# Kernel optimization log

Measured on AMD Instinct MI355X. Metric: run time of the kernel, lower is better.

Reference implementation:

```python
import jax, jax.numpy as jnp
import numpy as np

LN_EPS = 1e-5

def _layer_norm(y, g, b):
    mu = y.mean(-1, keepdims=True)
    var = y.var(-1, keepdims=True)
    return (y - mu) * jax.lax.rsqrt(var + LN_EPS) * g + b

def setup_inputs() -> dict:
    key = jax.random.key(0)
    ks = jax.random.split(key, 10)
    F, D, H = 32, 128, 128
    FD = F * D
    B = 8192
    def rn(k, shape, fan_in):
        return jax.random.normal(k, shape, dtype=jnp.float32) / np.sqrt(fan_in)
    return {
        "x":   jax.random.normal(ks[0], (B, F), dtype=jnp.float32),
        "Wp":  rn(ks[1], (F, D), 1), "bp": jnp.zeros((F, D), jnp.float32),
        "fW1": rn(ks[2], (F, D, H), D), "fb1": jnp.zeros((F, H), jnp.float32),
        "fW2": rn(ks[3], (F, H, D), H), "fb2": jnp.zeros((F, D), jnp.float32),
        "fWg": rn(ks[4], (F, D, 2 * D), D), "fbg": jnp.zeros((F, 2 * D), jnp.float32),
        "fg":  jnp.ones((F, D), jnp.float32), "fbe": jnp.zeros((F, D), jnp.float32),
        "sW1": rn(ks[5], (FD, H), FD), "sb1": jnp.zeros((H,), jnp.float32),
        "sW2": rn(ks[6], (H, FD), H), "sb2": jnp.zeros((FD,), jnp.float32),
        "sWg": rn(ks[7], (FD, 2 * FD), FD), "sbg": jnp.zeros((2 * FD,), jnp.float32),
        "sg":  jnp.ones((FD,), jnp.float32), "sbe": jnp.zeros((FD,), jnp.float32),
        "Wh":  rn(ks[8], (FD, F), FD), "bh": jnp.zeros((F,), jnp.float32),
    }

def reference(x, Wp, bp, fW1, fb1, fW2, fb2, fWg, fbg, fg, fbe,
              sW1, sb1, sW2, sb2, sWg, sbg, sg, sbe, Wh, bh):
    B, F = x.shape
    D = Wp.shape[1]
    # per-feature Linear(1, d_model), batched over all features: (B, F, D)
    emb = x[:, :, None] * Wp[None] + bp[None]
    # per-feature GRNs, batched via einsum over the feature axis
    h = jax.nn.elu(jnp.einsum('bfd,fdh->bfh', emb, fW1) + fb1)
    h = jnp.einsum('bfh,fhd->bfd', h, fW2) + fb2
    gates = jnp.einsum('bfd,fde->bfe', h, fWg) + fbg          # (B, F, 2D)
    a, s = jnp.split(gates, 2, axis=-1)
    stacked = _layer_norm(emb + a * jax.nn.sigmoid(s), fg, fbe)  # (B, F, D)
    # selection GRN over the flattened embeddings
    flat = stacked.reshape(B, F * D)
    hh = jax.nn.elu(flat @ sW1 + sb1)
    hh = hh @ sW2 + sb2
    sgate = flat_gate = hh @ sWg + sbg                          # (B, 2FD)
    sa, ss = jnp.split(sgate, 2, axis=-1)
    sel_in = _layer_norm(flat + sa * jax.nn.sigmoid(ss), sg, sbe)
    weights = jax.nn.softmax(sel_in @ Wh + bh, axis=-1)        # (B, F)
    selected = jnp.einsum('bfd,bf->bd', stacked, weights)      # (B, D)
    return selected, weights
```

## Files before the change

### kernel.cpp

```cpp
#include <hip/hip_runtime.h>
#include <hip/hip_bf16.h>
#include <math.h>

#define BB 8192
#define FF 32
#define DD 128
#define HH 128
#define FD 4096
#define E2 256
#define F2 8192
#define LN_EPS 1e-5f
#define L2E 1.44269504f
#define KSPLIT 8

typedef __hip_bfloat16 bf16;
typedef __attribute__((ext_vector_type(8))) short bf16x8;
typedef __attribute__((ext_vector_type(4))) float f32x4;

__device__ __forceinline__ float s2f(short s) {
  union { float f; unsigned u; } x; x.u = ((unsigned)(unsigned short)s) << 16; return x.f;
}
__device__ __forceinline__ short f2s(float v) {
  bf16 h = __float2bfloat16(v); return *(short*)&h;
}
__device__ __forceinline__ float fast_sigmoid(float s) {
  return __builtin_amdgcn_rcpf(1.f + __builtin_amdgcn_exp2f(-L2E * s));
}
__device__ __forceinline__ float fast_elu(float v) {
  return v > 0.f ? v : __builtin_amdgcn_exp2f(L2E * v) - 1.f;
}

__device__ __forceinline__ int swz64(int row, int hb) {
  return row * 128 + (hb ^ ((row & 7) << 4));
}


__global__ void prep_A1(const float* __restrict__ Wp, const float* __restrict__ bp,
                        const float* __restrict__ fW1, const float* __restrict__ fb1,
                        float* __restrict__ A1, float* __restrict__ C1) {
  int f = blockIdx.x, h = threadIdx.x;
  const float* w1 = fW1 + (size_t)f * DD * HH;
  float a = 0.f, c = 0.f;
  for (int d = 0; d < DD; ++d) {
    float w = w1[d * HH + h];
    a += Wp[f * DD + d] * w;
    c += bp[f * DD + d] * w;
  }
  A1[f * HH + h] = a;
  C1[f * HH + h] = c + fb1[f * HH + h];
}

__global__ void prep_M2(const float* __restrict__ fW2, const float* __restrict__ fWg,
                        float* __restrict__ M2) {
  int f = blockIdx.x, h = blockIdx.y, e = threadIdx.x;
  const float* w2 = fW2 + ((size_t)f * HH + h) * DD;
  const float* wg = fWg + (size_t)f * DD * E2;
  float acc = 0.f;
  for (int d = 0; d < DD; ++d) acc += w2[d] * wg[d * E2 + e];
  M2[((size_t)f * HH + h) * E2 + e] = acc;
}

__global__ void m2_castT(const float* __restrict__ M2, short* __restrict__ M2T) {
  __shared__ float T[64][65];
  int h0 = blockIdx.x * 64, e0 = blockIdx.y * 64, f = blockIdx.z;
  int t = threadIdx.x;
  for (int i = 0; i < 4; ++i) {
    int lin = t + 256 * i;
    int r = lin >> 4, c4 = (lin & 15) * 4;
    f32x4 v = *(const f32x4*)&M2[((size_t)f * HH + h0 + r) * E2 + e0 + c4];
    T[r][c4] = v[0]; T[r][c4 + 1] = v[1]; T[r][c4 + 2] = v[2]; T[r][c4 + 3] = v[3];
  }
  __syncthreads();
  for (int i = 0; i < 2; ++i) {
    int lin = t + 256 * i;
    int e = lin >> 3, h8 = (lin & 7) * 8;
    short o[8];
    for (int k = 0; k < 8; ++k) o[k] = f2s(T[h8 + k][e]);
    *(bf16x8*)&M2T[((size_t)f * E2 + e0 + e) * HH + h0 + h8] = *(bf16x8*)&o[0];
  }
}

__global__ void prep_c2(const float* __restrict__ fb2, const float* __restrict__ fWg,
                        const float* __restrict__ fbg, float* __restrict__ c2) {
  int f = blockIdx.x, e = threadIdx.x;
  const float* wg = fWg + (size_t)f * DD * E2;
  float acc = 0.f;
  for (int d = 0; d < DD; ++d) acc += fb2[f * DD + d] * wg[d * E2 + e];
  c2[f * E2 + e] = acc + fbg[f * E2 + e];
}

__global__ void cast_bf16(const float* __restrict__ in, short* __restrict__ out, int n) {
  int i = blockIdx.x * 256 + threadIdx.x;
  if (i < n) out[i] = f2s(in[i]);
}

__global__ void castT(const float* __restrict__ in, short* __restrict__ out, int R, int C) {
  __shared__ float T[64][65];
  int c0 = blockIdx.x * 64, r0 = blockIdx.y * 64;
  int t = threadIdx.x;
  for (int i = 0; i < 4; ++i) {
    int lin = t + 256 * i;
    int r = lin >> 4, c4 = (lin & 15) * 4;
    f32x4 v = *(const f32x4*)&in[(size_t)(r0 + r) * C + c0 + c4];
    T[r][c4] = v[0]; T[r][c4 + 1] = v[1]; T[r][c4 + 2] = v[2]; T[r][c4 + 3] = v[3];
  }
  __syncthreads();
  for (int i = 0; i < 2; ++i) {
    int lin = t + 256 * i;
    int c = lin >> 3, r8 = (lin & 7) * 8;
    short o[8];
    for (int e = 0; e < 8; ++e) o[e] = f2s(T[r8 + e][c]);
    *(bf16x8*)&out[(size_t)(c0 + c) * R + r0 + r8] = *(bf16x8*)&o[0];
  }
}

__global__ void init_misc(const float* __restrict__ sbg, const float* __restrict__ bh,
                          float* __restrict__ c3, float* __restrict__ rowstats,
                          float* __restrict__ u, float* __restrict__ w0) {
  int j = blockIdx.x * 256 + threadIdx.x;
  c3[j] = sbg[j];
  rowstats[2 * j] = 0.f;
  rowstats[2 * j + 1] = 0.f;
  if (j < 32) { u[j] = 0.f; w0[j] = bh[j]; }
}

__global__ void castT_c3(const float* __restrict__ in, short* __restrict__ out,
                         const float* __restrict__ sb2, float* __restrict__ c3) {
  __shared__ float T[64][65];
  int c0 = blockIdx.x * 64, r0 = blockIdx.y * 64;
  int t = threadIdx.x;
  for (int i = 0; i < 4; ++i) {
    int lin = t + 256 * i;
    int r = lin >> 4, c4 = (lin & 15) * 4;
    f32x4 v = *(const f32x4*)&in[(size_t)(r0 + r) * F2 + c0 + c4];
    T[r][c4] = v[0]; T[r][c4 + 1] = v[1]; T[r][c4 + 2] = v[2]; T[r][c4 + 3] = v[3];
  }
  __syncthreads();
  for (int i = 0; i < 2; ++i) {
    int lin = t + 256 * i;
    int c = lin >> 3, r8 = (lin & 7) * 8;
    short o[8];
    for (int e = 0; e < 8; ++e) o[e] = f2s(T[r8 + e][c]);
    *(bf16x8*)&out[(size_t)(c0 + c) * FD + r0 + r8] = *(bf16x8*)&o[0];
  }
  if (t < 64) {
    float s = 0.f;
    for (int r = 0; r < 64; ++r) s += sb2[r0 + r] * T[r][t];
    atomicAdd(&c3[c0 + t], s);
  }
}

__global__ void prep_whs(const float* __restrict__ Wh, const float* __restrict__ sg,
                         const float* __restrict__ sbe, short* __restrict__ WhS,
                         float* __restrict__ u, float* __restrict__ w0) {
  __shared__ float T[64][33];
  int k0 = blockIdx.x * 64;
  int t = threadIdx.x;
  {
    int k = t >> 5, c = t & 31;
    for (int i = 0; i < 8; ++i)
      T[k + 8 * i][c] = Wh[(size_t)(k0 + k + 8 * i) * FF + c];
  }
  __syncthreads();
  {
    int c = t >> 3, kk = (t & 7) * 8;
    short o[8];
    for (int i = 0; i < 8; ++i) o[i] = f2s(sg[k0 + kk + i] * T[kk + i][c]);
    *(bf16x8*)&WhS[(size_t)c * FD + k0 + kk] = *(bf16x8*)&o[0];
  }
  if (t < 32) {
    float su = 0.f, sw = 0.f;
    for (int k = 0; k < 64; ++k) { su += sg[k0 + k] * T[k][t]; sw += sbe[k0 + k] * T[k][t]; }
    atomicAdd(&u[t], su);
    atomicAdd(&w0[t], sw);
  }
}

__global__ __launch_bounds__(256) void gemm_bt_n128_splitk(
    const short* __restrict__ A, const short* __restrict__ BT,
    float* __restrict__ Cp, int M, int K) {
  __shared__ short As[128 * 72];
  __shared__ short Bs[128 * 72];
  int m0 = blockIdx.x * 128;
  int kchunk = K >> 3;
  int kbase = blockIdx.y * kchunk;
  int tid = threadIdx.x;
  int lane = tid & 63, w = tid >> 6;
  int wm = (w >> 1) * 64, wn = (w & 1) * 64;
  int lm = lane & 15, lq = lane >> 4;
  f32x4 acc[4][4] = {};
  for (int kc = 0; kc < kchunk; kc += 64) {
    for (int i = 0; i < 4; ++i) {
      int li = tid + 256 * i;
      int r = li >> 3, c8 = (li & 7) * 8;
      *(bf16x8*)&As[r * 72 + c8] = *(const bf16x8*)&A[(size_t)(m0 + r) * K + kbase + kc + c8];
      *(bf16x8*)&Bs[r * 72 + c8] = *(const bf16x8*)&BT[(size_t)r * K + kbase + kc + c8];
    }
    __syncthreads();
    for (int ks = 0; ks < 2; ++ks) {
      bf16x8 af[4], bfr[4];
      for (int i = 0; i < 4; ++i)
        af[i] = *(const bf16x8*)&As[(wm + i * 16 + lm) * 72 + ks * 32 + lq * 8];
      for (int j = 0; j < 4; ++j)
        bfr[j] = *(const bf16x8*)&Bs[(wn + j * 16 + lm) * 72 + ks * 32 + lq * 8];
      for (int i = 0; i < 4; ++i)
        for (int j = 0; j < 4; ++j)
          acc[i][j] = __builtin_amdgcn_mfma_f32_16x16x32_bf16(af[i], bfr[j], acc[i][j], 0, 0, 0);
    }
    __syncthreads();
  }
  float* out = Cp + (size_t)blockIdx.y * M * 128;
  for (int i = 0; i < 4; ++i)
    for (int j = 0; j < 4; ++j)
      for (int v = 0; v < 4; ++v) {
        int r = wm + i * 16 + lq * 4 + v;
        int c = wn + j * 16 + lm;
        out[(size_t)(m0 + r) * 128 + c] = acc[i][j][v];
      }
}

__global__ void reduce_m3t(const float* __restrict__ Cp, short* __restrict__ M3T, int M) {
  size_t i = (size_t)blockIdx.x * 256 + threadIdx.x;
  float s = 0.f;
  for (int k = 0; k < KSPLIT; ++k) s += Cp[(size_t)k * M * 128 + i];
  M3T[i] = f2s(s);
}

__global__ void reduce_hh1(const float* __restrict__ Cp, const float* __restrict__ sb1,
                           short* __restrict__ hh1, int M) {
  size_t i = (size_t)blockIdx.x * 256 + threadIdx.x;
  float s = 0.f;
  for (int k = 0; k < KSPLIT; ++k) s += Cp[(size_t)k * M * 128 + i];
  s += sb1[i & 127];
  hh1[i] = f2s(fast_elu(s));
}

__global__ __launch_bounds__(256) void stageA_mfma(
    const float* __restrict__ x, const float* __restrict__ Wp,
    const float* __restrict__ bp, const float* __restrict__ A1,
    const float* __restrict__ C1, const short* __restrict__ M2T,
    const float* __restrict__ c2, const float* __restrict__ fg,
    const float* __restrict__ fbe, short* __restrict__ stacked) {
  __shared__ __align__(16) char SM[(64 + 128) * 128];
  char* As = SM;
  char* Bs = SM + 64 * 128;
  short* Co = (short*)(SM + 64 * 128);
  float* red = (float*)SM;
  __shared__ float xsh[64];
  int f = blockIdx.y;
  int m0 = blockIdx.x * 64;
  int tid = threadIdx.x;
  int lane = tid & 63, w = tid >> 6;
  int wm = (w >> 1) * 32, wn = (w & 1) * 64;
  int lm = lane & 15, lq = lane >> 4;
  if (tid < 64) xsh[tid] = x[(size_t)(m0 + tid) * FF + f];
  __syncthreads();
  f32x4 accA[2][4] = {}, accB[2][4] = {};
  int c8 = (tid & 7) * 8, rb = tid >> 3;
  for (int kc = 0; kc < HH; kc += 64) {
    {
      f32x4 a1lo = *(const f32x4*)&A1[f * HH + kc + c8];
      f32x4 a1hi = *(const f32x4*)&A1[f * HH + kc + c8 + 4];
      f32x4 c1lo = *(const f32x4*)&C1[f * HH + kc + c8];
      f32x4 c1hi = *(const f32x4*)&C1[f * HH + kc + c8 + 4];
      for (int rr = 0; rr < 2; ++rr) {
        int row = rb + rr * 32;
        float xr = xsh[row];
        short o[8];
        for (int e = 0; e < 4; ++e) {
          o[e]     = f2s(fast_elu(fmaf(xr, a1lo[e], c1lo[e])));
          o[e + 4] = f2s(fast_elu(fmaf(xr, a1hi[e], c1hi[e])));
        }
        *(bf16x8*)(As + swz64(row, c8 * 2)) = *(bf16x8*)&o[0];
      }
    }
    for (int i = 0; i < 4; ++i) {
      int li = tid + 256 * i;
      int r = li >> 3, cc = (li & 7) * 8;
      bf16x8 va = *(const bf16x8*)&M2T[((size_t)f * E2 + r) * HH + kc + cc];
      *(bf16x8*)(Bs + swz64(r, cc * 2)) = va;
    }
    __syncthreads();
    bf16x8 af[2][2];
    for (int ks = 0; ks < 2; ++ks)
      for (int i = 0; i < 2; ++i)
        af[ks][i] = *(const bf16x8*)(As + swz64(wm + i * 16 + lm, ks * 64 + lq * 16));
    for (int ks = 0; ks < 2; ++ks) {
      int hb = ks * 64 + lq * 16;
      for (int j = 0; j < 4; ++j) {
        bf16x8 ba = *(const bf16x8*)(Bs + swz64(wn + j * 16 + lm, hb));
        for (int i = 0; i < 2; ++i)
          accA[i][j] = __builtin_amdgcn_mfma_f32_16x16x32_bf16(af[ks][i], ba, accA[i][j], 0, 0, 0);
      }
    }
    __syncthreads();
    for (int i = 0; i < 4; ++i) {
      int li = tid + 256 * i;
      int r = li >> 3, cc = (li & 7) * 8;
      bf16x8 vb = *(const bf16x8*)&M2T[((size_t)f * E2 + 128 + r) * HH + kc + cc];
      *(bf16x8*)(Bs + swz64(r, cc * 2)) = vb;
    }
    __syncthreads();
    for (int ks = 0; ks < 2; ++ks) {
      int hb = ks * 64 + lq * 16;
      for (int j = 0; j < 4; ++j) {
        bf16x8 bb = *(const bf16x8*)(Bs + swz64(wn + j * 16 + lm, hb));
        for (int i = 0; i < 2; ++i)
          accB[i][j] = __builtin_amdgcn_mfma_f32_16x16x32_bf16(af[ks][i], bb, accB[i][j], 0, 0, 0);
      }
    }
    __syncthreads();
  }
  float c2a[4], c2s[4], wpv[4], bpv[4];
  for (int j = 0; j < 4; ++j) {
    int c = wn + j * 16 + lm;
    c2a[j] = c2[f * E2 + c];
    c2s[j] = c2[f * E2 + 128 + c];
    wpv[j] = Wp[f * DD + c];
    bpv[j] = bp[f * DD + c];
  }
  float rs[2][4], rq[2][4];
  for (int i = 0; i < 2; ++i)
    for (int v = 0; v < 4; ++v) {
      int r = wm + i * 16 + lq * 4 + v;
      float xr = xsh[r];
      float sum = 0.f, sq = 0.f;
      for (int j = 0; j < 4; ++j) {
        float a = accA[i][j][v] + c2a[j];
        float s = accB[i][j][v] + c2s[j];
        float emb = fmaf(xr, wpv[j], bpv[j]);
        float y = fmaf(a, fast_sigmoid(s), emb);
        accA[i][j][v] = y;
        sum += y; sq += y * y;
      }
      rs[i][v] = sum; rq[i][v] = sq;
    }
  for (int m = 1; m < 16; m <<= 1)
    for (int i = 0; i < 2; ++i)
      for (int v = 0; v < 4; ++v) {
        rs[i][v] += __shfl_xor(rs[i][v], m, 64);
        rq[i][v] += __shfl_xor(rq[i][v], m, 64);
      }
  if (lm == 0)
    for (int i = 0; i < 2; ++i)
      for (int v = 0; v < 4; ++v) {
        int r = wm + i * 16 + lq * 4 + v;
        red[(w & 1) * 128 + r * 2]     = rs[i][v];
        red[(w & 1) * 128 + r * 2 + 1] = rq[i][v];
      }
  __syncthreads();
  float fgv[4], fbev[4];
  for (int j = 0; j < 4; ++j) {
    int c = wn + j * 16 + lm;
    fgv[j] = fg[f * DD + c];
    fbev[j] = fbe[f * DD + c];
  }
  for (int i = 0; i < 2; ++i)
    for (int v = 0; v < 4; ++v) {
      int r = wm + i * 16 + lq * 4 + v;
      float tot  = red[r * 2]     + red[128 + r * 2];
      float totq = red[r * 2 + 1] + red[128 + r * 2 + 1];
      float mu = tot * (1.f / DD);
      float var = totq * (1.f / DD) - mu * mu;
      float rstd = rsqrtf(var + LN_EPS);
      for (int j = 0; j < 4; ++j) {
        int c = wn + j * 16 + lm;
        Co[r * 128 + c] = f2s((accA[i][j][v] - mu) * rstd * fgv[j] + fbev[j]);
      }
    }
  __syncthreads();
  for (int i = 0; i < 4; ++i) {
    int lin = tid + 256 * i;
    int r = lin >> 4, cc8 = (lin & 15) * 8;
    *(bf16x8*)&stacked[((size_t)(m0 + r) * FF + f) * DD + cc8] = *(bf16x8*)&Co[r * 128 + cc8];
  }
}

__global__ __launch_bounds__(256) void sgate_mfma(
    const short* __restrict__ hh1, const short* __restrict__ M3T,
    const float* __restrict__ c3, const short* __restrict__ stacked,
    short* __restrict__ tmp, float* __restrict__ rowstats) {
  __shared__ short As[128 * 72];
  __shared__ short Ba[64 * 72];
  __shared__ short Bb[64 * 72];
  short* Co = As;
  int m0 = blockIdx.x * 128;
  int c0 = blockIdx.y * 64;
  int tid = threadIdx.x;
  int lane = tid & 63, w = tid >> 6;
  int wm = (w >> 1) * 64, wn = (w & 1) * 32;
  int lm = lane & 15, lq = lane >> 4;
  f32x4 accA[4][2] = {}, accB[4][2] = {};
  for (int kc = 0; kc < 128; kc += 64) {
    for (int i = 0; i < 4; ++i) {
      int li = tid + 256 * i;
      int r = li >> 3, c8 = (li & 7) * 8;
      *(bf16x8*)&As[r * 72 + c8] = *(const bf16x8*)&hh1[(size_t)(m0 + r) * 128 + kc + c8];
    }
    for (int i = 0; i < 2; ++i) {
      int li = tid + 256 * i;
      int r = li >> 3, c8 = (li & 7) * 8;
      *(bf16x8*)&Ba[r * 72 + c8] = *(const bf16x8*)&M3T[(size_t)(c0 + r) * 128 + kc + c8];
      *(bf16x8*)&Bb[r * 72 + c8] = *(const bf16x8*)&M3T[(size_t)(4096 + c0 + r) * 128 + kc + c8];
    }
    __syncthreads();
    for (int ks = 0; ks < 2; ++ks) {
      bf16x8 af[4], ba[2], bb[2];
      for (int i = 0; i < 4; ++i)
        af[i] = *(const bf16x8*)&As[(wm + i * 16 + lm) * 72 + ks * 32 + lq * 8];
      for (int j = 0; j < 2; ++j) {
        ba[j] = *(const bf16x8*)&Ba[(wn + j * 16 + lm) * 72 + ks * 32 + lq * 8];
        bb[j] = *(const bf16x8*)&Bb[(wn + j * 16 + lm) * 72 + ks * 32 + lq * 8];
      }
      for (int i = 0; i < 4; ++i)
        for (int j = 0; j < 2; ++j) {
          accA[i][j] = __builtin_amdgcn_mfma_f32_16x16x32_bf16(af[i], ba[j], accA[i][j], 0, 0, 0);
          accB[i][j] = __builtin_amdgcn_mfma_f32_16x16x32_bf16(af[i], bb[j], accB[i][j], 0, 0, 0);
        }
    }
    __syncthreads();
  }
  for (int i = 0; i < 4; ++i)
    for (int j = 0; j < 2; ++j)
      for (int v = 0; v < 4; ++v) {
        int rl = wm + i * 16 + lq * 4 + v;
        int cl = wn + j * 16 + lm;
        int c = c0 + cl;
        float sa = accA[i][j][v] + c3[c];
        float ss = accB[i][j][v] + c3[c + 4096];
        Co[rl * 64 + cl] = f2s(sa * fast_sigmoid(ss));
      }
  __syncthreads();
  for (int i = 0; i < 4; ++i) {
    int lin = tid + 256 * i;
    int r = lin >> 3, c8 = (lin & 7) * 8;
    size_t gi = (size_t)(m0 + r) * FD + c0 + c8;
    bf16x8 sv = *(const bf16x8*)&stacked[gi];
    bf16x8 av = *(bf16x8*)&Co[r * 64 + c8];
    short ov[8];
    float ps = 0.f, pq = 0.f;
    for (int e = 0; e < 8; ++e) {
      short o = f2s(s2f(sv[e]) + s2f(av[e]));
      ov[e] = o;
      float vb = s2f(o);
      ps += vb; pq += vb * vb;
    }
    *(bf16x8*)&tmp[gi] = *(bf16x8*)&ov[0];
    ps += __shfl_xor(ps, 1, 64); pq += __shfl_xor(pq, 1, 64);
    ps += __shfl_xor(ps, 2, 64); pq += __shfl_xor(pq, 2, 64);
    ps += __shfl_xor(ps, 4, 64); pq += __shfl_xor(pq, 4, 64);
    if ((tid & 7) == 0) {
      atomicAdd(&rowstats[2 * (m0 + r)], ps);
      atomicAdd(&rowstats[2 * (m0 + r) + 1], pq);
    }
  }
}

__global__ __launch_bounds__(256) void gemm_logits_splitk(
    const short* __restrict__ tmp, const short* __restrict__ WhS,
    float* __restrict__ partial) {
  __shared__ short As[128 * 72];
  __shared__ short Bs[32 * 72];
  int m0 = blockIdx.x * 128;
  int kbase = blockIdx.y * (FD / 8);
  int tid = threadIdx.x;
  int lane = tid & 63, w = tid >> 6;
  int wm = w * 32;
  int lm = lane & 15, lq = lane >> 4;
  f32x4 acc[2][2] = {};
  for (int kc = 0; kc < FD / 8; kc += 64) {
    for (int i = 0; i < 4; ++i) {
      int li = tid + 256 * i;
      int r = li >> 3, c8 = (li & 7) * 8;
      *(bf16x8*)&As[r * 72 + c8] = *(const bf16x8*)&tmp[(size_t)(m0 + r) * FD + kbase + kc + c8];
    }
    {
      int r = tid >> 3, c8 = (tid & 7) * 8;
      if (r < 32)
        *(bf16x8*)&Bs[r * 72 + c8] = *(const bf16x8*)&WhS[(size_t)r * FD + kbase + kc + c8];
    }
    __syncthreads();
    for (int ks = 0; ks < 2; ++ks) {
      bf16x8 af[2], bfr[2];
      for (int i = 0; i < 2; ++i)
        af[i] = *(const bf16x8*)&As[(wm + i * 16 + lm) * 72 + ks * 32 + lq * 8];
      for (int j = 0; j < 2; ++j)
        bfr[j] = *(const bf16x8*)&Bs[(j * 16 + lm) * 72 + ks * 32 + lq * 8];
      for (int i = 0; i < 2; ++i)
        for (int j = 0; j < 2; ++j)
          acc[i][j] = __builtin_amdgcn_mfma_f32_16x16x32_bf16(af[i], bfr[j], acc[i][j], 0, 0, 0);
    }
    __syncthreads();
  }
  for (int i = 0; i < 2; ++i)
    for (int j = 0; j < 2; ++j)
      for (int v = 0; v < 4; ++v) {
        int r = m0 + wm + i * 16 + lq * 4 + v;
        int c = j * 16 + lm;
        partial[(size_t)blockIdx.y * BB * FF + (size_t)r * FF + c] = acc[i][j][v];
      }
}

__global__ __launch_bounds__(128) void select_fused(
    const float* __restrict__ partial, const float* __restrict__ rowstats,
    const float* __restrict__ u, const float* __restrict__ w0,
    const short* __restrict__ stacked, float* __restrict__ outsel,
    float* __restrict__ outw) {
  __shared__ float wf[FF];
  __shared__ short L[FD];
  int b = blockIdx.x;
  int t = threadIdx.x;
  for (int i = 0; i < 4; ++i) {
    int idx = t + 128 * i;
    *(bf16x8*)&L[idx * 8] = *(const bf16x8*)&stacked[(size_t)b * FD + idx * 8];
  }
  if (t < 32) {
    float s = 0.f;
    for (int p = 0; p < KSPLIT; ++p) s += partial[(size_t)p * BB * FF + (size_t)b * FF + t];
    float tot  = rowstats[2 * b];
    float totq = rowstats[2 * b + 1];
    float mu = tot * (1.f / FD);
    float var = totq * (1.f / FD) - mu * mu;
    float rstd = rsqrtf(var + LN_EPS);
    float l = rstd * s - mu * rstd * u[t] + w0[t];
    float m = l;
    for (int off = 16; off; off >>= 1) m = fmaxf(m, __shfl_xor(m, off, 32));
    float e = __builtin_amdgcn_exp2f(L2E * (l - m));
    float ss = e;
    for (int off = 16; off; off >>= 1) ss += __shfl_xor(ss, off, 32);
    float wv = e / ss;
    wf[t] = wv;
    outw[(size_t)b * FF + t] = wv;
  }
  __syncthreads();
  float acc = 0.f;
  for (int ff = 0; ff < FF; ++ff) acc += s2f(L[ff * 128 + t]) * wf[ff];
  outsel[(size_t)b * DD + t] = acc;
}

extern "C" void kernel_launch(void* const* d_in, const int* in_sizes, int n_in,
                              void* d_out, int out_size, void* d_ws, size_t ws_size,
                              hipStream_t stream) {
  const float* x   = (const float*)d_in[0];
  const float* Wp  = (const float*)d_in[1];
  const float* bp  = (const float*)d_in[2];
  const float* fW1 = (const float*)d_in[3];
  const float* fb1 = (const float*)d_in[4];
  const float* fW2 = (const float*)d_in[5];
  const float* fb2 = (const float*)d_in[6];
  const float* fWg = (const float*)d_in[7];
  const float* fbg = (const float*)d_in[8];
  const float* fg  = (const float*)d_in[9];
  const float* fbe = (const float*)d_in[10];
  const float* sW1 = (const float*)d_in[11];
  const float* sb1 = (const float*)d_in[12];
  const float* sW2 = (const float*)d_in[13];
  const float* sb2 = (const float*)d_in[14];
  const float* sWg = (const float*)d_in[15];
  const float* sbg = (const float*)d_in[16];
  const float* sg  = (const float*)d_in[17];
  const float* sbe = (const float*)d_in[18];
  const float* Wh  = (const float*)d_in[19];
  const float* bh  = (const float*)d_in[20];

  float* w = (float*)d_ws;
  size_t off = 0;
  float* A1   = w + off; off += (size_t)FF * HH;
  float* C1   = w + off; off += (size_t)FF * HH;
  float* c2   = w + off; off += (size_t)FF * E2;
  float* c3   = w + off; off += (size_t)F2;
  float* rowstats = w + off; off += (size_t)2 * BB;
  float* u    = w + off; off += 32;
  float* w0   = w + off; off += 32;
  float* M2   = w + off; off += (size_t)FF * HH * E2;
  float* partial = w + off; off += (size_t)KSPLIT * BB * 128;
  short* hh1  = (short*)(w + off); off += (size_t)BB * 128 / 2;
  short* M3T  = (short*)(w + off); off += (size_t)F2 * 128 / 2;
  short* sW2b = (short*)(w + off); off += (size_t)128 * FD / 2;
  short* sW1T = (short*)(w + off); off += (size_t)128 * FD / 2;
  short* M2T  = (short*)(w + off); off += (size_t)FF * E2 * HH / 2;
  short* WhS  = (short*)(w + off); off += (size_t)FF * FD / 2;
  short* stacked = (short*)(w + off); off += (size_t)BB * FD / 2;
  short* tmp  = (short*)(w + off); off += (size_t)BB * FD / 2;
  short* sWgT = (short*)(w + off); off += (size_t)F2 * FD / 2;

  float* outsel = (float*)d_out;
  float* outw   = outsel + (size_t)BB * DD;

  cast_bf16<<<(128 * FD + 255) / 256, 256, 0, stream>>>(sW2, sW2b, 128 * FD);
  castT<<<dim3(DD / 64, FD / 64), 256, 0, stream>>>(sW1, sW1T, FD, DD);
  init_misc<<<F2 / 256, 256, 0, stream>>>(sbg, bh, c3, rowstats, u, w0);
  castT_c3<<<dim3(F2 / 64, FD / 64), 256, 0, stream>>>(sWg, sWgT, sb2, c3);
  prep_whs<<<FD / 64, 256, 0, stream>>>(Wh, sg, sbe, WhS, u, w0);
  gemm_bt_n128_splitk<<<dim3(F2 / 128, KSPLIT), 256, 0, stream>>>(sWgT, sW2b, partial, F2, FD);
  reduce_m3t<<<(F2 * 128) / 256, 256, 0, stream>>>(partial, M3T, F2);
  prep_A1<<<FF, 128, 0, stream>>>(Wp, bp, fW1, fb1, A1, C1);
  prep_M2<<<dim3(FF, HH), E2, 0, stream>>>(fW2, fWg, M2);
  m2_castT<<<dim3(HH / 64, E2 / 64, FF), 256, 0, stream>>>(M2, M2T);
  prep_c2<<<FF, E2, 0, stream>>>(fb2, fWg, fbg, c2);
  stageA_mfma<<<dim3(BB / 64, FF), 256, 0, stream>>>(x, Wp, bp, A1, C1, M2T, c2, fg, fbe,
                                                     stacked);
  gemm_bt_n128_splitk<<<dim3(BB / 128, KSPLIT), 256, 0, stream>>>(stacked, sW1T, partial, BB, FD);
  reduce_hh1<<<(BB * 128) / 256, 256, 0, stream>>>(partial, sb1, hh1, BB);
  sgate_mfma<<<dim3(BB / 128, FD / 64), 256, 0, stream>>>(hh1, M3T, c3, stacked, tmp, rowstats);
  gemm_logits_splitk<<<dim3(BB / 128, KSPLIT), 256, 0, stream>>>(tmp, WhS, partial);
  select_fused<<<BB, 128, 0, stream>>>(partial, rowstats, u, w0, stacked, outsel, outw);
}
```

Baseline: 505.3 us.

## Fuse logits GEMM into sgate epilogue with atomic slice accumulation

The separate split-K logits GEMM is removed. Each sgate block now multiplies its bf16 residual tile, kept in swizzled shared memory, by the matching 64-wide slice of WhS and atomically adds the partial logits into one of eight slice buffers. This avoids writing and re-reading the full B×FD tmp tensor and drops one kernel launch. In exchange it adds many float atomics and a larger zero-init, and summation order now varies from run to run.

```diff
diff --git a/kernel.cpp b/kernel.cpp
--- a/kernel.cpp
+++ b/kernel.cpp
@@ -12,6 +12,7 @@
 #define LN_EPS 1e-5f
 #define L2E 1.44269504f
 #define KSPLIT 8
+#define LSLICE 8
 
 typedef __hip_bfloat16 bf16;
 typedef __attribute__((ext_vector_type(8))) short bf16x8;
@@ -32,6 +33,9 @@
 
 __device__ __forceinline__ int swz64(int row, int hb) {
   return row * 128 + (hb ^ ((row & 7) << 4));
+}
+__device__ __forceinline__ int swzs(int row, int cs) {
+  return row * 64 + (cs ^ ((row & 7) << 3));
 }
 
 
@@ -116,11 +120,12 @@
 
 __global__ void init_misc(const float* __restrict__ sbg, const float* __restrict__ bh,
                           float* __restrict__ c3, float* __restrict__ rowstats,
-                          float* __restrict__ u, float* __restrict__ w0) {
+                          float* __restrict__ u, float* __restrict__ w0,
+                          float* __restrict__ lpart) {
   int j = blockIdx.x * 256 + threadIdx.x;
-  c3[j] = sbg[j];
-  rowstats[2 * j] = 0.f;
-  rowstats[2 * j + 1] = 0.f;
+  lpart[j] = 0.f;
+  if (j < F2) c3[j] = sbg[j];
+  if (j < 2 * BB) rowstats[j] = 0.f;
   if (j < 32) { u[j] = 0.f; w0[j] = bh[j]; }
 }
 
@@ -379,11 +384,13 @@
 __global__ __launch_bounds__(256) void sgate_mfma(
     const short* __restrict__ hh1, const short* __restrict__ M3T,
     const float* __restrict__ c3, const short* __restrict__ stacked,
-    short* __restrict__ tmp, float* __restrict__ rowstats) {
+    const short* __restrict__ WhS, float* __restrict__ rowstats,
+    float* __restrict__ lpart) {
   __shared__ short As[128 * 72];
   __shared__ short Ba[64 * 72];
   __shared__ short Bb[64 * 72];
   short* Co = As;
+  short* Bw = Ba;
   int m0 = blockIdx.x * 128;
   int c0 = blockIdx.y * 64;
   int tid = threadIdx.x;
@@ -428,7 +435,7 @@
         int c = c0 + cl;
         float sa = accA[i][j][v] + c3[c];
         float ss = accB[i][j][v] + c3[c + 4096];
-        Co[rl * 64 + cl] = f2s(sa * fast_sigmoid(ss));
+        Co[swzs(rl, cl)] = f2s(sa * fast_sigmoid(ss));
       }
   __syncthreads();
   for (int i = 0; i < 4; ++i) {
@@ -436,7 +443,8 @@
     int r = lin >> 3, c8 = (lin & 7) * 8;
     size_t gi = (size_t)(m0 + r) * FD + c0 + c8;
     bf16x8 sv = *(const bf16x8*)&stacked[gi];
-    bf16x8 av = *(bf16x8*)&Co[r * 64 + c8];
+    int ci = swzs(r, c8);
+    bf16x8 av = *(bf16x8*)&Co[ci];
     short ov[8];
     float ps = 0.f, pq = 0.f;
     for (int e = 0; e < 8; ++e) {
@@ -445,7 +453,7 @@
       float vb = s2f(o);
       ps += vb; pq += vb * vb;
     }
-    *(bf16x8*)&tmp[gi] = *(bf16x8*)&ov[0];
+    *(bf16x8*)&Co[ci] = *(bf16x8*)&ov[0];
     ps += __shfl_xor(ps, 1, 64); pq += __shfl_xor(pq, 1, 64);
     ps += __shfl_xor(ps, 2, 64); pq += __shfl_xor(pq, 2, 64);
     ps += __shfl_xor(ps, 4, 64); pq += __shfl_xor(pq, 4, 64);
@@ -454,55 +462,39 @@
       atomicAdd(&rowstats[2 * (m0 + r) + 1], pq);
     }
   }
-}
-
-__global__ __launch_bounds__(256) void gemm_logits_splitk(
-    const short* __restrict__ tmp, const short* __restrict__ WhS,
-    float* __restrict__ partial) {
-  __shared__ short As[128 * 72];
-  __shared__ short Bs[32 * 72];
-  int m0 = blockIdx.x * 128;
-  int kbase = blockIdx.y * (FD / 8);
-  int tid = threadIdx.x;
-  int lane = tid & 63, w = tid >> 6;
-  int wm = w * 32;
-  int lm = lane & 15, lq = lane >> 4;
-  f32x4 acc[2][2] = {};
-  for (int kc = 0; kc < FD / 8; kc += 64) {
-    for (int i = 0; i < 4; ++i) {
-      int li = tid + 256 * i;
-      int r = li >> 3, c8 = (li & 7) * 8;
-      *(bf16x8*)&As[r * 72 + c8] = *(const bf16x8*)&tmp[(size_t)(m0 + r) * FD + kbase + kc + c8];
-    }
-    {
-      int r = tid >> 3, c8 = (tid & 7) * 8;
-      if (r < 32)
-        *(bf16x8*)&Bs[r * 72 + c8] = *(const bf16x8*)&WhS[(size_t)r * FD + kbase + kc + c8];
-    }
-    __syncthreads();
+  {
+    int r = tid >> 3, c8 = (tid & 7) * 8;
+    *(bf16x8*)&Bw[r * 72 + c8] = *(const bf16x8*)&WhS[(size_t)r * FD + c0 + c8];
+  }
+  __syncthreads();
+  {
+    int wm2 = w * 32;
+    f32x4 lacc[2][2] = {};
     for (int ks = 0; ks < 2; ++ks) {
-      bf16x8 af[2], bfr[2];
-      for (int i = 0; i < 2; ++i)
-        af[i] = *(const bf16x8*)&As[(wm + i * 16 + lm) * 72 + ks * 32 + lq * 8];
+      bf16x8 af2[2], bf2[2];
+      for (int i = 0; i < 2; ++i) {
+        int rr = wm2 + i * 16 + lm;
+        af2[i] = *(const bf16x8*)&Co[swzs(rr, ks * 32 + lq * 8)];
+      }
       for (int j = 0; j < 2; ++j)
-        bfr[j] = *(const bf16x8*)&Bs[(j * 16 + lm) * 72 + ks * 32 + lq * 8];
+        bf2[j] = *(const bf16x8*)&Bw[(j * 16 + lm) * 72 + ks * 32 + lq * 8];
       for (int i = 0; i < 2; ++i)
         for (int j = 0; j < 2; ++j)
-          acc[i][j] = __builtin_amdgcn_mfma_f32_16x16x32_bf16(af[i], bfr[j], acc[i][j], 0, 0, 0);
-    }
-    __syncthreads();
-  }
-  for (int i = 0; i < 2; ++i)
-    for (int j = 0; j < 2; ++j)
-      for (int v = 0; v < 4; ++v) {
-        int r = m0 + wm + i * 16 + lq * 4 + v;
-        int c = j * 16 + lm;
-        partial[(size_t)blockIdx.y * BB * FF + (size_t)r * FF + c] = acc[i][j][v];
-      }
+          lacc[i][j] = __builtin_amdgcn_mfma_f32_16x16x32_bf16(af2[i], bf2[j], lacc[i][j], 0, 0, 0);
+    }
+    float* lp = lpart + (size_t)(blockIdx.y & (LSLICE - 1)) * BB * FF;
+    for (int i = 0; i < 2; ++i)
+      for (int j = 0; j < 2; ++j)
+        for (int v = 0; v < 4; ++v) {
+          int r = wm2 + i * 16 + lq * 4 + v;
+          int c = j * 16 + lm;
+          atomicAdd(&lp[(size_t)(m0 + r) * FF + c], lacc[i][j][v]);
+        }
+  }
 }
 
 __global__ __launch_bounds__(128) void select_fused(
-    const float* __restrict__ partial, const float* __restrict__ rowstats,
+    const float* __restrict__ lpart, const float* __restrict__ rowstats,
     const float* __restrict__ u, const float* __restrict__ w0,
     const short* __restrict__ stacked, float* __restrict__ outsel,
     float* __restrict__ outw) {
@@ -516,7 +508,7 @@
   }
   if (t < 32) {
     float s = 0.f;
-    for (int p = 0; p < KSPLIT; ++p) s += partial[(size_t)p * BB * FF + (size_t)b * FF + t];
+    for (int p = 0; p < LSLICE; ++p) s += lpart[(size_t)p * BB * FF + (size_t)b * FF + t];
     float tot  = rowstats[2 * b];
     float totq = rowstats[2 * b + 1];
     float mu = tot * (1.f / FD);
@@ -574,6 +566,7 @@
   float* w0   = w + off; off += 32;
   float* M2   = w + off; off += (size_t)FF * HH * E2;
   float* partial = w + off; off += (size_t)KSPLIT * BB * 128;
+  float* lpart = w + off; off += (size_t)LSLICE * BB * FF;
   short* hh1  = (short*)(w + off); off += (size_t)BB * 128 / 2;
   short* M3T  = (short*)(w + off); off += (size_t)F2 * 128 / 2;
   short* sW2b = (short*)(w + off); off += (size_t)128 * FD / 2;
@@ -581,7 +574,6 @@
   short* M2T  = (short*)(w + off); off += (size_t)FF * E2 * HH / 2;
   short* WhS  = (short*)(w + off); off += (size_t)FF * FD / 2;
   short* stacked = (short*)(w + off); off += (size_t)BB * FD / 2;
-  short* tmp  = (short*)(w + off); off += (size_t)BB * FD / 2;
   short* sWgT = (short*)(w + off); off += (size_t)F2 * FD / 2;
 
   float* outsel = (float*)d_out;
@@ -589,7 +581,7 @@
 
   cast_bf16<<<(128 * FD + 255) / 256, 256, 0, stream>>>(sW2, sW2b, 128 * FD);
   castT<<<dim3(DD / 64, FD / 64), 256, 0, stream>>>(sW1, sW1T, FD, DD);
-  init_misc<<<F2 / 256, 256, 0, stream>>>(sbg, bh, c3, rowstats, u, w0);
+  init_misc<<<(LSLICE * BB * FF) / 256, 256, 0, stream>>>(sbg, bh, c3, rowstats, u, w0, lpart);
   castT_c3<<<dim3(F2 / 64, FD / 64), 256, 0, stream>>>(sWg, sWgT, sb2, c3);
   prep_whs<<<FD / 64, 256, 0, stream>>>(Wh, sg, sbe, WhS, u, w0);
   gemm_bt_n128_splitk<<<dim3(F2 / 128, KSPLIT), 256, 0, stream>>>(sWgT, sW2b, partial, F2, FD);
@@ -602,7 +594,7 @@
                                                      stacked);
   gemm_bt_n128_splitk<<<dim3(BB / 128, KSPLIT), 256, 0, stream>>>(stacked, sW1T, partial, BB, FD);
   reduce_hh1<<<(BB * 128) / 256, 256, 0, stream>>>(partial, sb1, hh1, BB);
-  sgate_mfma<<<dim3(BB / 128, FD / 64), 256, 0, stream>>>(hh1, M3T, c3, stacked, tmp, rowstats);
-  gemm_logits_splitk<<<dim3(BB / 128, KSPLIT), 256, 0, stream>>>(tmp, WhS, partial);
-  select_fused<<<BB, 128, 0, stream>>>(partial, rowstats, u, w0, stacked, outsel, outw);
-}
+  sgate_mfma<<<dim3(BB / 128, FD / 64), 256, 0, stream>>>(hh1, M3T, c3, stacked, WhS,
+                                                          rowstats, lpart);
+  select_fused<<<BB, 128, 0, stream>>>(lpart, rowstats, u, w0, stacked, outsel, outw);
+}
```

After: 512.4 us. Within noise of the previous version (+1.4%).
